# Optimization experiments

Hardware: AMD Instinct MI355X
Metric: run time of the kernel (lower is better)

The kernel has to match this reference:

```python
import jax, jax.numpy as jnp
import numpy as np

N, E, ATOM, HID, H, OUT, NCLS, G = 30000, 480000, 128, 128, 4, 256, 2, 64
NEG = 0.2  # LeakyReLU slope (both GATConv internal and self.relu)


def _ln(x, g, b):
    mu = x.mean(-1, keepdims=True)
    v = ((x - mu) ** 2).mean(-1, keepdims=True)
    return g * (x - mu) * jax.lax.rsqrt(v + 1e-5) + b


def _lrelu(x, s=NEG):
    return jnp.where(x >= 0, x, s * x)


def _gat(x, src, dst, W, a_s, a_d, b, concat, n):
    # PyG GATConv: h = W x (per head); alpha_e = softmax_dst(LeakyReLU(a_s.h_src + a_d.h_dst))
    h = (x @ W).reshape(n, H, -1)                      # [N,H,C]
    e = _lrelu((h * a_s).sum(-1)[src] + (h * a_d).sum(-1)[dst])  # [E,H]
    m = jax.ops.segment_max(e, dst, num_segments=n)
    m = jnp.where(jnp.isfinite(m), m, 0.0)
    ex = jnp.exp(e - m[dst])
    den = jax.ops.segment_sum(ex, dst, num_segments=n)
    alpha = ex / den[dst]                              # per-destination softmax
    out = jax.ops.segment_sum(h[src] * alpha[:, :, None], dst, num_segments=n)
    out = out.reshape(n, -1) if concat else out.mean(1)
    return out + b, alpha


def setup_inputs() -> dict:
    key = jax.random.key(0)
    ks = jax.random.split(key, 16)
    def w(k, shape, fan):
        return jax.random.normal(k, shape, jnp.float32) / np.sqrt(fan).astype(np.float32)
    return dict(
        x=jax.random.normal(ks[0], (N, ATOM), jnp.float32),
        edge_index=jax.random.randint(ks[1], (2, E), 0, N),
        batch=jnp.sort(jax.random.randint(ks[2], (N,), 0, G)),
        W1=w(ks[3], (ATOM, H * HID), ATOM),
        as1=w(ks[4], (H, HID), HID), ad1=w(ks[5], (H, HID), HID),
        b1=jnp.zeros((HID,), jnp.float32),
        g_ln=jnp.ones((HID,), jnp.float32), b_ln=jnp.zeros((HID,), jnp.float32),
        W2=w(ks[6], (HID, H * HID), HID),
        as2=w(ks[7], (H, HID), HID), ad2=w(ks[8], (H, HID), HID),
        b2=jnp.zeros((H * HID,), jnp.float32),
        Wl0=w(ks[9], (H * HID, HID), H * HID), bl0=jnp.zeros((HID,), jnp.float32),
        Ws1=w(ks[10], (HID, OUT), HID), bs1=jnp.zeros((OUT,), jnp.float32),
        g1=jnp.ones((OUT,), jnp.float32), bb1=jnp.zeros((OUT,), jnp.float32),
        Ws2=w(ks[11], (OUT, OUT // 2), OUT), bs2=jnp.zeros((OUT // 2,), jnp.float32),
        g2=jnp.ones((OUT // 2,), jnp.float32), bb2=jnp.zeros((OUT // 2,), jnp.float32),
        Ws3=w(ks[12], (OUT // 2, NCLS), OUT // 2), bs3=jnp.zeros((NCLS,), jnp.float32),
    )


def reference(x, edge_index, batch, W1, as1, ad1, b1, g_ln, b_ln, W2, as2, ad2, b2, Wl0, bl0, Ws1, bs1, g1, bb1, Ws2, bs2, g2, bb2, Ws3, bs3):
    n = x.shape[0]
    loop = jnp.arange(n)
    src = jnp.concatenate([edge_index[0], loop])  # PyG adds self loops
    dst = jnp.concatenate([edge_index[1], loop])
    h, _ = _gat(x, src, dst, W1, as1, ad1, b1, False, n)      # concat=False -> head mean
    h = _lrelu(_ln(h, g_ln, b_ln))
    h, alpha = _gat(h, src, dst, W2, as2, ad2, b2, True, n)   # concat=True -> [N, H*HID]
    h = _lrelu(h)
    pooled = jax.ops.segment_sum(h, batch, num_segments=G)
    cnt = jax.ops.segment_sum(jnp.ones((n,), h.dtype), batch, num_segments=G)
    pooled = pooled / jnp.maximum(cnt, 1.0)[:, None]          # global_mean_pool
    z = pooled @ Wl0 + bl0
    z = jax.nn.relu(_ln(z @ Ws1 + bs1, g1, bb1))              # dropout = identity (eval)
    z = jax.nn.relu(_ln(z @ Ws2 + bs2, g2, bb2))
    probs = jax.nn.softmax(z @ Ws3 + bs3, axis=-1)
    return probs, alpha
```

## Files before the change

### kernel.cpp

```cpp
#include <hip/hip_runtime.h>
#include <cstdint>
#include <cstddef>


typedef __attribute__((ext_vector_type(8))) short bf16x8;
typedef __attribute__((ext_vector_type(4))) float f32x4;

__device__ __forceinline__ float lrelu(float v) { return v >= 0.f ? v : 0.2f * v; }

__device__ __forceinline__ float4 lrelu4(float4 v) {
    return make_float4(lrelu(v.x), lrelu(v.y), lrelu(v.z), lrelu(v.w));
}
__device__ __forceinline__ float4 add4(float4 a, float4 b) {
    return make_float4(a.x + b.x, a.y + b.y, a.z + b.z, a.w + b.w);
}

__device__ __forceinline__ unsigned short f2bf(float x) {
    unsigned int u = __float_as_uint(x);
    u += 0x7FFFu + ((u >> 16) & 1u);
    return (unsigned short)(u >> 16);
}

__global__ void cvt_bf16_k(const float* __restrict__ src,
                           unsigned short* __restrict__ dst, int n4) {
    int i = blockIdx.x * 256 + threadIdx.x;
    if (i >= n4) return;
    float4 v = *(const float4*)&src[i * 4];
    ushort4 o;
    o.x = f2bf(v.x); o.y = f2bf(v.y); o.z = f2bf(v.z); o.w = f2bf(v.w);
    *(ushort4*)&dst[i * 4] = o;
}

__global__ void cvt_wt_k(const float* __restrict__ W1, const float* __restrict__ W2,
                         unsigned short* __restrict__ Wt1, unsigned short* __restrict__ Wt2) {
    const float* W = blockIdx.z ? W2 : W1;
    unsigned short* Wt = blockIdx.z ? Wt2 : Wt1;
    int head = blockIdx.y;
    int idx = blockIdx.x * 256 + threadIdx.x;
    int k = idx >> 7, c = idx & 127;
    Wt[((size_t)head * 128 + c) * 128 + k] = f2bf(W[(size_t)k * 512 + head * 128 + c]);
}

__global__ __launch_bounds__(256) void gemm_mfma(const unsigned short* __restrict__ Abf,
                                                 const unsigned short* __restrict__ Wbt,
                                                 unsigned short* __restrict__ hbout,
                                                 const float* __restrict__ a_s,
                                                 const float* __restrict__ a_d,
                                                 float* __restrict__ ssrc,
                                                 float* __restrict__ sdst, int M) {
    __shared__ unsigned short Als[64][136];
    __shared__ unsigned short Bls[128][136];
    const int tid = threadIdx.x;
    const int row0 = blockIdx.x * 64;
    const int head = blockIdx.y;

#pragma unroll
    for (int i = 0; i < 4; i++) {
        int c = tid + i * 256;
        int r = c >> 4, k0 = (c & 15) * 8;
        uint4 v = make_uint4(0, 0, 0, 0);
        int gr = row0 + r;
        if (gr < M) v = *(const uint4*)&Abf[(size_t)gr * 128 + k0];
        *(uint4*)&Als[r][k0] = v;
    }
    const unsigned short* Wh = Wbt + (size_t)head * 128 * 128;
#pragma unroll
    for (int i = 0; i < 8; i++) {
        int c = tid + i * 256;
        int col = c >> 4, k0 = (c & 15) * 8;
        *(uint4*)&Bls[col][k0] = *(const uint4*)&Wh[col * 128 + k0];
    }
    __syncthreads();

    const int w = tid >> 6, l = tid & 63;
    const int li = l & 15, lg = l >> 4;

    f32x4 acc[8] = {};
#pragma unroll
    for (int kt = 0; kt < 4; kt++) {
        bf16x8 a = *(const bf16x8*)&Als[w * 16 + li][kt * 32 + lg * 8];
#pragma unroll
        for (int ct = 0; ct < 8; ct++) {
            bf16x8 b = *(const bf16x8*)&Bls[ct * 16 + li][kt * 32 + lg * 8];
            acc[ct] = __builtin_amdgcn_mfma_f32_16x16x32_bf16(a, b, acc[ct], 0, 0, 0);
        }
    }

#pragma unroll
    for (int ct = 0; ct < 8; ct++) {
#pragma unroll
        for (int r = 0; r < 4; r++) {
            int gr = row0 + w * 16 + lg * 4 + r;
            if (gr < M)
                hbout[(size_t)gr * 512 + head * 128 + ct * 16 + li] = f2bf(acc[ct][r]);
        }
    }

    float ps[4] = {}, pd[4] = {};
#pragma unroll
    for (int ct = 0; ct < 8; ct++) {
        float as_v = a_s[head * 128 + ct * 16 + li];
        float ad_v = a_d[head * 128 + ct * 16 + li];
#pragma unroll
        for (int r = 0; r < 4; r++) { ps[r] += acc[ct][r] * as_v; pd[r] += acc[ct][r] * ad_v; }
    }
#pragma unroll
    for (int o = 1; o <= 8; o <<= 1) {
#pragma unroll
        for (int r = 0; r < 4; r++) { ps[r] += __shfl_xor(ps[r], o); pd[r] += __shfl_xor(pd[r], o); }
    }
    if (li == 0) {
#pragma unroll
        for (int r = 0; r < 4; r++) {
            int gr = row0 + w * 16 + lg * 4 + r;
            if (gr < M) { ssrc[gr * 4 + head] = ps[r]; sdst[gr * 4 + head] = pd[r]; }
        }
    }
}

__global__ void hist_k(const int* __restrict__ ei, int E, int ET, int* __restrict__ deg) {
    int e = blockIdx.x * 256 + threadIdx.x;
    if (e >= ET) return;
    int d = (e < E) ? ei[E + e] : e - E;
    atomicAdd(&deg[d], 1);
}

__global__ __launch_bounds__(1024) void scan_k(const int* __restrict__ deg,
                                               int* __restrict__ rowptr,
                                               int* __restrict__ cursor, int Nn) {
    __shared__ int part[1024];
    int t = threadIdx.x;
    int per = (Nn + 1023) / 1024;
    int b0 = t * per, b1 = min(b0 + per, Nn);
    int s = 0;
    for (int i = b0; i < b1; i++) s += deg[i];
    part[t] = s;
    __syncthreads();
    for (int o = 1; o < 1024; o <<= 1) {
        int x = (t >= o) ? part[t - o] : 0;
        __syncthreads();
        part[t] += x;
        __syncthreads();
    }
    int off = part[t] - s;
    for (int i = b0; i < b1; i++) {
        rowptr[i] = off; cursor[i] = off; off += deg[i];
    }
    if (t == 1023) rowptr[Nn] = part[1023];
}

__global__ void fill_csr_k(const int* __restrict__ ei, int E, int ET,
                           int* __restrict__ cursor,
                           int* __restrict__ csr_src, int* __restrict__ csr_eid) {
    int e = blockIdx.x * 256 + threadIdx.x;
    if (e >= ET) return;
    int s, d;
    if (e < E) { s = ei[e]; d = ei[E + e]; } else { s = d = e - E; }
    int pos = atomicAdd(&cursor[d], 1);
    csr_src[pos] = s;
    csr_eid[pos] = e;
}

__global__ __launch_bounds__(256) void gat_agg(const int* __restrict__ rowptr,
                                               const int* __restrict__ csr_src,
                                               const int* __restrict__ csr_eid,
                                               const float4* __restrict__ ssrc,
                                               const float4* __restrict__ sdst,
                                               const unsigned short* __restrict__ hb,
                                               float* __restrict__ out,
                                               unsigned short* __restrict__ outb,
                                               float4* __restrict__ aout,
                                               const float* __restrict__ b1,
                                               const float* __restrict__ gln,
                                               const float* __restrict__ bln,
                                               int Nn, int concat) {
    __shared__ float alds[4][64][4];
    const int lane = threadIdx.x & 63;
    const int w = threadIdx.x >> 6;
    const int d = blockIdx.x * 4 + w;
    if (d >= Nn) return;
    const int beg = rowptr[d], end = rowptr[d + 1];
    const float4 sd = sdst[d];
    const float NINF = -__builtin_huge_valf();

    float4 m = make_float4(NINF, NINF, NINF, NINF);
    for (int i = beg + lane; i < end; i += 64) {
        float4 ev = lrelu4(add4(ssrc[csr_src[i]], sd));
        m.x = fmaxf(m.x, ev.x); m.y = fmaxf(m.y, ev.y);
        m.z = fmaxf(m.z, ev.z); m.w = fmaxf(m.w, ev.w);
    }
    for (int o = 32; o; o >>= 1) {
        m.x = fmaxf(m.x, __shfl_xor(m.x, o));
        m.y = fmaxf(m.y, __shfl_xor(m.y, o));
        m.z = fmaxf(m.z, __shfl_xor(m.z, o));
        m.w = fmaxf(m.w, __shfl_xor(m.w, o));
    }

    float4 den = make_float4(0.f, 0.f, 0.f, 0.f);
    for (int i = beg + lane; i < end; i += 64) {
        float4 ev = lrelu4(add4(ssrc[csr_src[i]], sd));
        den.x += __expf(ev.x - m.x); den.y += __expf(ev.y - m.y);
        den.z += __expf(ev.z - m.z); den.w += __expf(ev.w - m.w);
    }
    for (int o = 32; o; o >>= 1) {
        den.x += __shfl_xor(den.x, o);
        den.y += __shfl_xor(den.y, o);
        den.z += __shfl_xor(den.z, o);
        den.w += __shfl_xor(den.w, o);
    }
    float4 inv;
    inv.x = 1.f / den.x; inv.y = 1.f / den.y;
    inv.z = 1.f / den.z; inv.w = 1.f / den.w;

    const int head = lane >> 4;
    float acc[8] = {};
    for (int chunk = beg; chunk < end; chunk += 64) {
        const int n = min(64, end - chunk);
        if (lane < n) {
            int i = chunk + lane;
            float4 ev = lrelu4(add4(ssrc[csr_src[i]], sd));
            float4 a4;
            a4.x = __expf(ev.x - m.x) * inv.x;
            a4.y = __expf(ev.y - m.y) * inv.y;
            a4.z = __expf(ev.z - m.z) * inv.z;
            a4.w = __expf(ev.w - m.w) * inv.w;
            alds[w][lane][0] = a4.x; alds[w][lane][1] = a4.y;
            alds[w][lane][2] = a4.z; alds[w][lane][3] = a4.w;
            if (aout != nullptr) aout[csr_eid[i]] = a4;
        }
        for (int j = 0; j < n; ++j) {
            int s = csr_src[chunk + j];
            float a = alds[w][j][head];
            uint4 q = *(const uint4*)(hb + (size_t)s * 512 + lane * 8);
            acc[0] += a * __uint_as_float(q.x << 16);
            acc[1] += a * __uint_as_float(q.x & 0xFFFF0000u);
            acc[2] += a * __uint_as_float(q.y << 16);
            acc[3] += a * __uint_as_float(q.y & 0xFFFF0000u);
            acc[4] += a * __uint_as_float(q.z << 16);
            acc[5] += a * __uint_as_float(q.z & 0xFFFF0000u);
            acc[6] += a * __uint_as_float(q.w << 16);
            acc[7] += a * __uint_as_float(q.w & 0xFFFF0000u);
        }
    }

    if (concat) {
        float4* orow = (float4*)(out + (size_t)d * 512 + lane * 8);
        orow[0] = make_float4(acc[0], acc[1], acc[2], acc[3]);
        orow[1] = make_float4(acc[4], acc[5], acc[6], acc[7]);
    } else {
#pragma unroll
        for (int k = 0; k < 8; k++) acc[k] += __shfl_xor(acc[k], 16);
#pragma unroll
        for (int k = 0; k < 8; k++) acc[k] += __shfl_xor(acc[k], 32);
        const int c0 = (lane & 15) * 8;
        float val[8];
        float s = 0.f;
#pragma unroll
        for (int k = 0; k < 8; k++) { val[k] = 0.25f * acc[k] + b1[c0 + k]; s += val[k]; }
#pragma unroll
        for (int o = 1; o <= 8; o <<= 1) s += __shfl_xor(s, o);
        float mu = s * (1.f / 128.f);
        float v = 0.f;
#pragma unroll
        for (int k = 0; k < 8; k++) { float dk = val[k] - mu; v += dk * dk; }
#pragma unroll
        for (int o = 1; o <= 8; o <<= 1) v += __shfl_xor(v, o);
        float r = rsqrtf(v * (1.f / 128.f) + 1e-5f);
        if (lane < 16) {
            unsigned int u[4];
#pragma unroll
            for (int k = 0; k < 4; k++) {
                float y0 = lrelu(gln[c0 + 2 * k]     * (val[2 * k]     - mu) * r + bln[c0 + 2 * k]);
                float y1 = lrelu(gln[c0 + 2 * k + 1] * (val[2 * k + 1] - mu) * r + bln[c0 + 2 * k + 1]);
                u[k] = (unsigned int)f2bf(y0) | ((unsigned int)f2bf(y1) << 16);
            }
            *(uint4*)&outb[(size_t)d * 128 + c0] = make_uint4(u[0], u[1], u[2], u[3]);
        }
    }
}

__global__ __launch_bounds__(512) void pool_k(const float* __restrict__ out2,
                                              const float* __restrict__ b2,
                                              const int* __restrict__ batch,
                                              float* __restrict__ pooled, int Nn) {
    int c = threadIdx.x;
    int n0 = blockIdx.x * 64, n1 = min(n0 + 64, Nn);
    if (n0 >= Nn) return;
    float bc = b2[c];
    int g = batch[n0];
    float acc = 0.f;
    for (int n = n0; n < n1; ++n) {
        int bg = batch[n];
        if (bg != g) { atomicAdd(&pooled[g * 512 + c], acc); acc = 0.f; g = bg; }
        float v = out2[(size_t)n * 512 + c] + bc;
        acc += lrelu(v);
    }
    atomicAdd(&pooled[g * 512 + c], acc);
}

__device__ __forceinline__ float block_sum(float v, volatile float* sbuf, int tid, int nw) {
    for (int o = 32; o; o >>= 1) v += __shfl_down(v, o);
    if ((tid & 63) == 0) sbuf[tid >> 6] = v;
    __syncthreads();
    if (tid == 0) { float r = 0.f; for (int i = 0; i < nw; i++) r += sbuf[i]; sbuf[0] = r; }
    __syncthreads();
    float r = sbuf[0];
    __syncthreads();
    return r;
}

__global__ __launch_bounds__(256) void mlp_head(const float* __restrict__ pooled,
                                                const int* __restrict__ batch, int Nn,
                                                const float* __restrict__ Wl0, const float* __restrict__ bl0,
                                                const float* __restrict__ Ws1, const float* __restrict__ bs1,
                                                const float* __restrict__ g1,  const float* __restrict__ bb1,
                                                const float* __restrict__ Ws2, const float* __restrict__ bs2,
                                                const float* __restrict__ g2,  const float* __restrict__ bb2,
                                                const float* __restrict__ Ws3, const float* __restrict__ bs3,
                                                float* __restrict__ probs) {
    __shared__ float z0[128], z1[256], z2[128];
    __shared__ float sbuf[8];
    const int g = blockIdx.x, t = threadIdx.x;

    int lo = 0, hi = Nn;
    while (lo < hi) { int mid = (lo + hi) >> 1; if (batch[mid] < g) lo = mid + 1; else hi = mid; }
    int a = lo;
    lo = 0; hi = Nn;
    while (lo < hi) { int mid = (lo + hi) >> 1; if (batch[mid] < g + 1) lo = mid + 1; else hi = mid; }
    float inv = 1.f / fmaxf((float)(lo - a), 1.f);

    if (t < 128) {
        float acc = 0.f;
        for (int k = 0; k < 512; k++) acc += pooled[g * 512 + k] * Wl0[k * 128 + t];
        z0[t] = acc * inv + bl0[t];
    }
    __syncthreads();

    {
        float acc = bs1[t];
        for (int k = 0; k < 128; k++) acc += z0[k] * Ws1[k * 256 + t];
        float mu = block_sum(acc, sbuf, t, 4) * (1.f / 256.f);
        float dd = acc - mu;
        float var = block_sum(dd * dd, sbuf, t, 4) * (1.f / 256.f);
        z1[t] = fmaxf(g1[t] * dd * rsqrtf(var + 1e-5f) + bb1[t], 0.f);
    }
    __syncthreads();

    {
        float acc = 0.f;
        if (t < 128) {
            acc = bs2[t];
            for (int k = 0; k < 256; k++) acc += z1[k] * Ws2[k * 128 + t];
        }
        float mu = block_sum(acc, sbuf, t, 4) * (1.f / 128.f);
        float dd = (t < 128) ? acc - mu : 0.f;
        float var = block_sum(dd * dd, sbuf, t, 4) * (1.f / 128.f);
        if (t < 128) z2[t] = fmaxf(g2[t] * dd * rsqrtf(var + 1e-5f) + bb2[t], 0.f);
    }
    __syncthreads();

    if (t == 0) {
        float p0 = bs3[0], p1 = bs3[1];
        for (int k = 0; k < 128; k++) { p0 += z2[k] * Ws3[k * 2]; p1 += z2[k] * Ws3[k * 2 + 1]; }
        float mx = fmaxf(p0, p1);
        float e0 = __expf(p0 - mx), e1 = __expf(p1 - mx);
        float s = e0 + e1;
        probs[g * 2 + 0] = e0 / s;
        probs[g * 2 + 1] = e1 / s;
    }
}

extern "C" void kernel_launch(void* const* d_in, const int* in_sizes, int n_in,
                              void* d_out, int out_size, void* d_ws, size_t ws_size,
                              hipStream_t stream) {
    const float* x    = (const float*)d_in[0];
    const int*   ei   = (const int*)d_in[1];
    const int*   batch= (const int*)d_in[2];
    const float* W1   = (const float*)d_in[3];
    const float* as1  = (const float*)d_in[4];
    const float* ad1  = (const float*)d_in[5];
    const float* b1   = (const float*)d_in[6];
    const float* g_ln = (const float*)d_in[7];
    const float* b_ln = (const float*)d_in[8];
    const float* W2   = (const float*)d_in[9];
    const float* as2  = (const float*)d_in[10];
    const float* ad2  = (const float*)d_in[11];
    const float* b2   = (const float*)d_in[12];
    const float* Wl0  = (const float*)d_in[13];
    const float* bl0  = (const float*)d_in[14];
    const float* Ws1  = (const float*)d_in[15];
    const float* bs1  = (const float*)d_in[16];
    const float* g1   = (const float*)d_in[17];
    const float* bb1  = (const float*)d_in[18];
    const float* Ws2  = (const float*)d_in[19];
    const float* bs2  = (const float*)d_in[20];
    const float* g2   = (const float*)d_in[21];
    const float* bb2  = (const float*)d_in[22];
    const float* Ws3  = (const float*)d_in[23];
    const float* bs3  = (const float*)d_in[24];
    (void)n_in; (void)out_size; (void)ws_size;

    const int Nn = in_sizes[0] / 128;
    const int E  = in_sizes[1] / 2;
    const int ET = E + Nn;
    const int G  = 64;

    char* ws = (char*)d_ws;
    size_t off = 0;
    auto alloc = [&](size_t bytes) { void* p = ws + off; off += (bytes + 255) & ~(size_t)255; return p; };
    unsigned short* hb   = (unsigned short*)alloc((size_t)Nn * 512 * 2);
    unsigned short* xb   = (unsigned short*)alloc((size_t)Nn * 128 * 2);
    unsigned short* hlnb = (unsigned short*)alloc((size_t)Nn * 128 * 2);
    unsigned short* Wbt1 = (unsigned short*)alloc((size_t)4 * 128 * 128 * 2);
    unsigned short* Wbt2 = (unsigned short*)alloc((size_t)4 * 128 * 128 * 2);
    float* out2   = (float*)alloc((size_t)Nn * 512 * 4);
    float* pooled = (float*)alloc((size_t)G * 512 * 4);
    float* ssrc   = (float*)alloc((size_t)Nn * 4 * 4);
    float* sdst   = (float*)alloc((size_t)Nn * 4 * 4);
    int*   deg    = (int*)alloc((size_t)Nn * 4);
    int*   rowptr = (int*)alloc((size_t)(Nn + 1) * 4);
    int*   cursor = (int*)alloc((size_t)Nn * 4);
    int*   csr_src= (int*)alloc((size_t)ET * 4);
    int*   csr_eid= (int*)alloc((size_t)ET * 4);

    float* probs = (float*)d_out;
    float* aout  = (float*)d_out + 128;

    hipMemsetAsync(deg, 0, (size_t)Nn * 4, stream);
    hipMemsetAsync(pooled, 0, (size_t)G * 512 * 4, stream);

    const int eblks = (ET + 255) / 256;
    dim3 ggrid((Nn + 63) / 64, 4);
    const int ablks = (Nn + 3) / 4;

    cvt_bf16_k<<<(Nn * 128 / 4 + 255) / 256, 256, 0, stream>>>(x, xb, Nn * 128 / 4);
    cvt_wt_k<<<dim3(64, 4, 2), 256, 0, stream>>>(W1, W2, Wbt1, Wbt2);

    hist_k<<<eblks, 256, 0, stream>>>(ei, E, ET, deg);
    scan_k<<<1, 1024, 0, stream>>>(deg, rowptr, cursor, Nn);
    fill_csr_k<<<eblks, 256, 0, stream>>>(ei, E, ET, cursor, csr_src, csr_eid);

    gemm_mfma<<<ggrid, 256, 0, stream>>>(xb, Wbt1, hb, as1, ad1, ssrc, sdst, Nn);
    gat_agg<<<ablks, 256, 0, stream>>>(rowptr, csr_src, csr_eid,
                                       (const float4*)ssrc, (const float4*)sdst,
                                       hb, nullptr, hlnb, nullptr, b1, g_ln, b_ln, Nn, 0);

    gemm_mfma<<<ggrid, 256, 0, stream>>>(hlnb, Wbt2, hb, as2, ad2, ssrc, sdst, Nn);
    gat_agg<<<ablks, 256, 0, stream>>>(rowptr, csr_src, csr_eid,
                                       (const float4*)ssrc, (const float4*)sdst,
                                       hb, out2, nullptr, (float4*)aout,
                                       nullptr, nullptr, nullptr, Nn, 1);

    pool_k<<<(Nn + 63) / 64, 512, 0, stream>>>(out2, b2, batch, pooled, Nn);
    mlp_head<<<G, 256, 0, stream>>>(pooled, batch, Nn, Wl0, bl0, Ws1, bs1, g1, bb1,
                                    Ws2, bs2, g2, bb2, Ws3, bs3, probs);
}
```

Measured before the change: 483.7 us.

## Fuse global mean pooling into second GAT aggregation, drop out2 buffer

The second gat_agg now applies bias and LeakyReLU in registers and accumulates per-graph sums directly into the pooled buffer. When all four destination nodes in a block share a graph it reduces through shared memory first, otherwise it falls back to per-lane global atomics. This removes the write and re-read of the 30000x512 fp32 out2 buffer and the separate pool kernel launch. In exchange it adds __syncthreads to gat_agg, more global atomics (a float atomic order that is nondeterministic), and an unroll-2 hint on the gather loop.

```diff
diff --git a/kernel.cpp b/kernel.cpp
--- a/kernel.cpp
+++ b/kernel.cpp
@@ -167,87 +167,120 @@
                                                const float4* __restrict__ ssrc,
                                                const float4* __restrict__ sdst,
                                                const unsigned short* __restrict__ hb,
-                                               float* __restrict__ out,
                                                unsigned short* __restrict__ outb,
                                                float4* __restrict__ aout,
                                                const float* __restrict__ b1,
                                                const float* __restrict__ gln,
                                                const float* __restrict__ bln,
+                                               const float* __restrict__ b2,
+                                               const int* __restrict__ batch,
+                                               float* __restrict__ pooled,
                                                int Nn, int concat) {
     __shared__ float alds[4][64][4];
-    const int lane = threadIdx.x & 63;
-    const int w = threadIdx.x >> 6;
+    __shared__ float pp[512];
+    __shared__ int gids[4];
+    const int t = threadIdx.x;
+    const int lane = t & 63;
+    const int w = t >> 6;
     const int d = blockIdx.x * 4 + w;
-    if (d >= Nn) return;
-    const int beg = rowptr[d], end = rowptr[d + 1];
-    const float4 sd = sdst[d];
-    const float NINF = -__builtin_huge_valf();
-
-    float4 m = make_float4(NINF, NINF, NINF, NINF);
-    for (int i = beg + lane; i < end; i += 64) {
-        float4 ev = lrelu4(add4(ssrc[csr_src[i]], sd));
-        m.x = fmaxf(m.x, ev.x); m.y = fmaxf(m.y, ev.y);
-        m.z = fmaxf(m.z, ev.z); m.w = fmaxf(m.w, ev.w);
-    }
-    for (int o = 32; o; o >>= 1) {
-        m.x = fmaxf(m.x, __shfl_xor(m.x, o));
-        m.y = fmaxf(m.y, __shfl_xor(m.y, o));
-        m.z = fmaxf(m.z, __shfl_xor(m.z, o));
-        m.w = fmaxf(m.w, __shfl_xor(m.w, o));
-    }
-
-    float4 den = make_float4(0.f, 0.f, 0.f, 0.f);
-    for (int i = beg + lane; i < end; i += 64) {
-        float4 ev = lrelu4(add4(ssrc[csr_src[i]], sd));
-        den.x += __expf(ev.x - m.x); den.y += __expf(ev.y - m.y);
-        den.z += __expf(ev.z - m.z); den.w += __expf(ev.w - m.w);
-    }
-    for (int o = 32; o; o >>= 1) {
-        den.x += __shfl_xor(den.x, o);
-        den.y += __shfl_xor(den.y, o);
-        den.z += __shfl_xor(den.z, o);
-        den.w += __shfl_xor(den.w, o);
-    }
-    float4 inv;
-    inv.x = 1.f / den.x; inv.y = 1.f / den.y;
-    inv.z = 1.f / den.z; inv.w = 1.f / den.w;
-
-    const int head = lane >> 4;
+    const bool active = d < Nn;
+
+    if (concat) {
+        pp[t] = 0.f; pp[t + 256] = 0.f;
+        if (lane == 0) gids[w] = active ? batch[d] : -1;
+    }
+    __syncthreads();
+
     float acc[8] = {};
-    for (int chunk = beg; chunk < end; chunk += 64) {
-        const int n = min(64, end - chunk);
-        if (lane < n) {
-            int i = chunk + lane;
+    if (active) {
+        const int beg = rowptr[d], end = rowptr[d + 1];
+        const float4 sd = sdst[d];
+        const float NINF = -__builtin_huge_valf();
+
+        float4 m = make_float4(NINF, NINF, NINF, NINF);
+        for (int i = beg + lane; i < end; i += 64) {
             float4 ev = lrelu4(add4(ssrc[csr_src[i]], sd));
-            float4 a4;
-            a4.x = __expf(ev.x - m.x) * inv.x;
-            a4.y = __expf(ev.y - m.y) * inv.y;
-            a4.z = __expf(ev.z - m.z) * inv.z;
-            a4.w = __expf(ev.w - m.w) * inv.w;
-            alds[w][lane][0] = a4.x; alds[w][lane][1] = a4.y;
-            alds[w][lane][2] = a4.z; alds[w][lane][3] = a4.w;
-            if (aout != nullptr) aout[csr_eid[i]] = a4;
-        }
-        for (int j = 0; j < n; ++j) {
-            int s = csr_src[chunk + j];
-            float a = alds[w][j][head];
-            uint4 q = *(const uint4*)(hb + (size_t)s * 512 + lane * 8);
-            acc[0] += a * __uint_as_float(q.x << 16);
-            acc[1] += a * __uint_as_float(q.x & 0xFFFF0000u);
-            acc[2] += a * __uint_as_float(q.y << 16);
-            acc[3] += a * __uint_as_float(q.y & 0xFFFF0000u);
-            acc[4] += a * __uint_as_float(q.z << 16);
-            acc[5] += a * __uint_as_float(q.z & 0xFFFF0000u);
-            acc[6] += a * __uint_as_float(q.w << 16);
-            acc[7] += a * __uint_as_float(q.w & 0xFFFF0000u);
+            m.x = fmaxf(m.x, ev.x); m.y = fmaxf(m.y, ev.y);
+            m.z = fmaxf(m.z, ev.z); m.w = fmaxf(m.w, ev.w);
+        }
+        for (int o = 32; o; o >>= 1) {
+            m.x = fmaxf(m.x, __shfl_xor(m.x, o));
+            m.y = fmaxf(m.y, __shfl_xor(m.y, o));
+            m.z = fmaxf(m.z, __shfl_xor(m.z, o));
+            m.w = fmaxf(m.w, __shfl_xor(m.w, o));
+        }
+
+        float4 den = make_float4(0.f, 0.f, 0.f, 0.f);
+        for (int i = beg + lane; i < end; i += 64) {
+            float4 ev = lrelu4(add4(ssrc[csr_src[i]], sd));
+            den.x += __expf(ev.x - m.x); den.y += __expf(ev.y - m.y);
+            den.z += __expf(ev.z - m.z); den.w += __expf(ev.w - m.w);
+        }
+        for (int o = 32; o; o >>= 1) {
+            den.x += __shfl_xor(den.x, o);
+            den.y += __shfl_xor(den.y, o);
+            den.z += __shfl_xor(den.z, o);
+            den.w += __shfl_xor(den.w, o);
+        }
+        float4 inv;
+        inv.x = 1.f / den.x; inv.y = 1.f / den.y;
+        inv.z = 1.f / den.z; inv.w = 1.f / den.w;
+
+        const int head = lane >> 4;
+        for (int chunk = beg; chunk < end; chunk += 64) {
+            const int n = min(64, end - chunk);
+            if (lane < n) {
+                int i = chunk + lane;
+                float4 ev = lrelu4(add4(ssrc[csr_src[i]], sd));
+                float4 a4;
+                a4.x = __expf(ev.x - m.x) * inv.x;
+                a4.y = __expf(ev.y - m.y) * inv.y;
+                a4.z = __expf(ev.z - m.z) * inv.z;
+                a4.w = __expf(ev.w - m.w) * inv.w;
+                alds[w][lane][0] = a4.x; alds[w][lane][1] = a4.y;
+                alds[w][lane][2] = a4.z; alds[w][lane][3] = a4.w;
+                if (concat) aout[csr_eid[i]] = a4;
+            }
+#pragma unroll 2
+            for (int j = 0; j < n; ++j) {
+                int s = csr_src[chunk + j];
+                float a = alds[w][j][head];
+                uint4 q = *(const uint4*)(hb + (size_t)s * 512 + lane * 8);
+                acc[0] += a * __uint_as_float(q.x << 16);
+                acc[1] += a * __uint_as_float(q.x & 0xFFFF0000u);
+                acc[2] += a * __uint_as_float(q.y << 16);
+                acc[3] += a * __uint_as_float(q.y & 0xFFFF0000u);
+                acc[4] += a * __uint_as_float(q.z << 16);
+                acc[5] += a * __uint_as_float(q.z & 0xFFFF0000u);
+                acc[6] += a * __uint_as_float(q.w << 16);
+                acc[7] += a * __uint_as_float(q.w & 0xFFFF0000u);
+            }
         }
     }
 
     if (concat) {
-        float4* orow = (float4*)(out + (size_t)d * 512 + lane * 8);
-        orow[0] = make_float4(acc[0], acc[1], acc[2], acc[3]);
-        orow[1] = make_float4(acc[4], acc[5], acc[6], acc[7]);
-    } else {
+        const int c0 = lane * 8;
+        float val[8];
+        if (active) {
+#pragma unroll
+            for (int k = 0; k < 8; k++) val[k] = lrelu(acc[k] + b2[c0 + k]);
+        }
+        const bool uniform = (gids[0] >= 0) && (gids[0] == gids[3]);
+        if (uniform && active) {
+#pragma unroll
+            for (int k = 0; k < 8; k++) atomicAdd(&pp[c0 + k], val[k]);
+        }
+        __syncthreads();
+        if (uniform) {
+            const int g0 = gids[0];
+            atomicAdd(&pooled[g0 * 512 + t], pp[t]);
+            atomicAdd(&pooled[g0 * 512 + t + 256], pp[t + 256]);
+        } else if (active) {
+            const int gw = gids[w];
+#pragma unroll
+            for (int k = 0; k < 8; k++) atomicAdd(&pooled[gw * 512 + c0 + k], val[k]);
+        }
+    } else if (active) {
 #pragma unroll
         for (int k = 0; k < 8; k++) acc[k] += __shfl_xor(acc[k], 16);
 #pragma unroll
@@ -277,25 +310,6 @@
             *(uint4*)&outb[(size_t)d * 128 + c0] = make_uint4(u[0], u[1], u[2], u[3]);
         }
     }
-}
-
-__global__ __launch_bounds__(512) void pool_k(const float* __restrict__ out2,
-                                              const float* __restrict__ b2,
-                                              const int* __restrict__ batch,
-                                              float* __restrict__ pooled, int Nn) {
-    int c = threadIdx.x;
-    int n0 = blockIdx.x * 64, n1 = min(n0 + 64, Nn);
-    if (n0 >= Nn) return;
-    float bc = b2[c];
-    int g = batch[n0];
-    float acc = 0.f;
-    for (int n = n0; n < n1; ++n) {
-        int bg = batch[n];
-        if (bg != g) { atomicAdd(&pooled[g * 512 + c], acc); acc = 0.f; g = bg; }
-        float v = out2[(size_t)n * 512 + c] + bc;
-        acc += lrelu(v);
-    }
-    atomicAdd(&pooled[g * 512 + c], acc);
 }
 
 __device__ __forceinline__ float block_sum(float v, volatile float* sbuf, int tid, int nw) {
@@ -413,7 +427,6 @@
     unsigned short* hlnb = (unsigned short*)alloc((size_t)Nn * 128 * 2);
     unsigned short* Wbt1 = (unsigned short*)alloc((size_t)4 * 128 * 128 * 2);
     unsigned short* Wbt2 = (unsigned short*)alloc((size_t)4 * 128 * 128 * 2);
-    float* out2   = (float*)alloc((size_t)Nn * 512 * 4);
     float* pooled = (float*)alloc((size_t)G * 512 * 4);
     float* ssrc   = (float*)alloc((size_t)Nn * 4 * 4);
     float* sdst   = (float*)alloc((size_t)Nn * 4 * 4);
@@ -443,15 +456,15 @@
     gemm_mfma<<<ggrid, 256, 0, stream>>>(xb, Wbt1, hb, as1, ad1, ssrc, sdst, Nn);
     gat_agg<<<ablks, 256, 0, stream>>>(rowptr, csr_src, csr_eid,
                                        (const float4*)ssrc, (const float4*)sdst,
-                                       hb, nullptr, hlnb, nullptr, b1, g_ln, b_ln, Nn, 0);
+                                       hb, hlnb, nullptr, b1, g_ln, b_ln,
+                                       nullptr, nullptr, nullptr, Nn, 0);
 
     gemm_mfma<<<ggrid, 256, 0, stream>>>(hlnb, Wbt2, hb, as2, ad2, ssrc, sdst, Nn);
     gat_agg<<<ablks, 256, 0, stream>>>(rowptr, csr_src, csr_eid,
                                        (const float4*)ssrc, (const float4*)sdst,
-                                       hb, out2, nullptr, (float4*)aout,
-                                       nullptr, nullptr, nullptr, Nn, 1);
-
-    pool_k<<<(Nn + 63) / 64, 512, 0, stream>>>(out2, b2, batch, pooled, Nn);
+                                       hb, nullptr, (float4*)aout, nullptr, nullptr, nullptr,
+                                       b2, batch, pooled, Nn, 1);
+
     mlp_head<<<G, 256, 0, stream>>>(pooled, batch, Nn, Wl0, bl0, Ws1, bs1, g1, bb1,
                                     Ws2, bs2, g2, bb2, Ws3, bs3, probs);
 }
```

New measurement: 510.8 us. 1.06x slower.
